# Performance work log

Measured on AMD Instinct MI355X. Metric: run time of the kernel, lower is better.

Reference implementation:

```python
import math
import jax, jax.numpy as jnp
import numpy as np

# module hyperparams (match init_kwargs)
EMBED = 1024
HEADS = 16
FACTOR = 3  # autocorrelation_factor


def setup_inputs() -> dict:
    key = jax.random.key(0)
    ks = jax.random.split(key, 9)
    B, T, E = 8, 4096, EMBED
    s = 1.0 / np.sqrt(E)
    inp = {"hidden_states": jax.random.normal(ks[0], (B, T, E), jnp.float32)}
    for i, n in enumerate(["q", "k", "v", "o"]):
        inp[f"W{n}"] = jax.random.normal(ks[1 + i], (E, E), jnp.float32) * s
        inp[f"b{n}"] = jax.random.normal(ks[5 + i], (E,), jnp.float32) * 0.01
    return inp


def reference(hidden_states, Wq, bq, Wk, bk, Wv, bv, Wo, bo):
    B, T, E = hidden_states.shape
    H = HEADS
    D = E // H  # head_dim

    def shape(x):  # [B,T,E] -> [B*H, T, D]
        return x.reshape(B, T, H, D).transpose(0, 2, 1, 3).reshape(B * H, T, D)

    q = shape(hidden_states @ Wq + bq)
    k = shape(hidden_states @ Wk + bk)
    v = shape(hidden_states @ Wv + bv)

    # FFT-based autocorrelation along the time axis: irfft(rfft(Q) * conj(rfft(K)))
    qf = jnp.fft.rfft(q, axis=1)
    kf = jnp.fft.rfft(k, axis=1)
    attn_weights = jnp.fft.irfft(qf * jnp.conj(kf), n=T, axis=1)  # [B*H, T, D]

    # mean over heads and channel -> [B, T]
    mean_ac = attn_weights.reshape(B, H, T, D).mean(axis=(1, 3))
    top_k = int(FACTOR * math.log(T))
    top_vals, top_idx = jax.lax.top_k(mean_ac, top_k)  # [B, K] each
    # NOTE: original code computes softmax of top_vals but (typo:
    # `top_k_autocrrelations`) never uses it; the raw autocorrelation values
    # are used as aggregation weights. We replicate that exactly.

    BN = B * H
    # torch `.repeat(num_heads, ...)` on a [bsz,1,1] tensor tiles the bsz block
    # num_heads times, so flat index bn maps to batch bn % B.
    bidx = jnp.arange(BN) % B
    w_flat = top_vals[bidx]  # [BN, K]
    d_flat = top_idx[bidx]   # [BN, K]

    t = jnp.arange(T)

    def body(acc, kd):
        d_k, w_k = kd  # [BN], [BN]
        # gather from doubled values == circular shift by delay
        idx = (t[None, :] + d_k[:, None]) % T  # [BN, T]
        rolled = jnp.take_along_axis(v, idx[:, :, None], axis=1)  # [BN, T, D]
        return acc + w_k[:, None, None] * rolled, None

    agg, _ = jax.lax.scan(body, jnp.zeros_like(v), (d_flat.T, w_flat.T))

    out = agg.reshape(B, H, T, D).transpose(0, 2, 1, 3).reshape(B, T, E)
    return out @ Wo + bo
```

## Files before the change

### kernel.cpp

```cpp
#include <hip/hip_runtime.h>


typedef unsigned short u16;
typedef __attribute__((ext_vector_type(8))) short short8_t;
typedef __attribute__((ext_vector_type(4))) float float4_t;

struct cplx { float x, y; };
struct __align__(8) u16x4 { u16 x, y, z, w; };

#define DEVINL static __device__ __forceinline__

DEVINL u16 bf_from_f(float x){
  unsigned u = __float_as_uint(x);
  u += 0x7fffu + ((u >> 16) & 1u);
  return (u16)(u >> 16);
}
DEVINL float f_from_bf(u16 h){ return __uint_as_float(((unsigned)h) << 16); }

DEVINL void nt_store_f(float* p, float v){ __builtin_nontemporal_store(v, p); }
DEVINL void nt_store_u16(u16* p, u16 v){ __builtin_nontemporal_store(v, p); }
DEVINL void nt_store_f4(float* p, float4_t v){ __builtin_nontemporal_store(v, (float4_t*)p); }

typedef const void __attribute__((address_space(1)))* gas_ptr;
typedef void __attribute__((address_space(3)))* las_ptr;
DEVINL void async16(const void* g, void* l){
  __builtin_amdgcn_global_load_lds((gas_ptr)g, (las_ptr)l, 16, 0, 0);
}


__global__ void k_split2(const float* __restrict__ Wq, const float* __restrict__ Wk,
                         u16* __restrict__ Qh, u16* __restrict__ Ql,
                         u16* __restrict__ Kh, u16* __restrict__ Kl){
  int isK = blockIdx.x >> 10;
  int i = (blockIdx.x & 1023) * 256 + threadIdx.x;
  const float* src = isK ? Wk : Wq;
  u16* ph = isK ? Kh : Qh;
  u16* pl = isK ? Kl : Ql;
  float4 v = ((const float4*)src)[i];
  u16x4 h, l;
  h.x = bf_from_f(v.x); l.x = bf_from_f(v.x - f_from_bf(h.x));
  h.y = bf_from_f(v.y); l.y = bf_from_f(v.y - f_from_bf(h.y));
  h.z = bf_from_f(v.z); l.z = bf_from_f(v.z - f_from_bf(h.z));
  h.w = bf_from_f(v.w); l.w = bf_from_f(v.w - f_from_bf(h.w));
  ((u16x4*)ph)[i] = h; ((u16x4*)pl)[i] = l;
}

__global__ void k_transpose2_bf16(const float* __restrict__ Wv, const float* __restrict__ Wo,
                                  u16* __restrict__ WvT, u16* __restrict__ WoT){
  __shared__ float tile[32][33];
  const float* W = blockIdx.z ? Wo : Wv;
  u16* WT = blockIdx.z ? WoT : WvT;
  int k0 = blockIdx.x * 32, n0 = blockIdx.y * 32;
  int x = threadIdx.x, y0 = threadIdx.y;
  for (int j = y0; j < 32; j += 8) tile[j][x] = W[(size_t)(k0 + j) * 1024 + n0 + x];
  __syncthreads();
  for (int j = y0; j < 32; j += 8) WT[(size_t)(n0 + j) * 1024 + k0 + x] = bf_from_f(tile[x][j]);
}

__global__ __launch_bounds__(256) void k_uvc(const float* __restrict__ Wq,
    const float* __restrict__ Wk, const float* __restrict__ bq, const float* __restrict__ bk,
    float* __restrict__ u, float* __restrict__ w2, float* __restrict__ c0){
  int gw = blockIdx.x * 4 + (threadIdx.x >> 6);
  int lane = threadIdx.x & 63;
  if (gw < 2048){
    const float* row = (gw < 1024) ? (Wq + (size_t)gw * 1024) : (Wk + (size_t)(gw - 1024) * 1024);
    const float* vec = (gw < 1024) ? bk : bq;
    float s = 0;
    for (int m = lane; m < 1024; m += 64) s += row[m] * vec[m];
    for (int o = 32; o; o >>= 1) s += __shfl_down(s, o);
    if (lane == 0){ if (gw < 1024) u[gw] = s; else w2[gw - 1024] = s; }
  } else if (gw == 2048){
    float s = 0;
    for (int m = lane; m < 1024; m += 64) s += bq[m] * bk[m];
    for (int o = 32; o; o >>= 1) s += __shfl_down(s, o);
    if (lane == 0) c0[0] = s;
  }
}

__global__ __launch_bounds__(256) void k_prep_hs(const float* __restrict__ hs,
    u16* __restrict__ hi, u16* __restrict__ lo, float* __restrict__ hsT,
    const float* __restrict__ uu, const float* __restrict__ w2,
    float* __restrict__ partQ, float* __restrict__ partK){
  __shared__ float tile[64][66];
  int b = blockIdx.z;
  int t0 = blockIdx.x * 64, e0 = blockIdx.y * 64;
  int tid = threadIdx.x;
  int eq = tid & 15;
  int tr = tid >> 4;
  const float* ib = hs + (size_t)b * 4194304;
  float4 u4 = *(const float4*)(uu + e0 + eq * 4);
  float4 w4 = *(const float4*)(w2 + e0 + eq * 4);
  float a1 = 0.f, a2 = 0.f;
  #pragma unroll
  for (int r = 0; r < 4; ++r){
    int t = tr + r * 16;
    size_t off = (size_t)(t0 + t) * 1024 + e0 + eq * 4;
    float4 v = *(const float4*)(ib + off);
    a1 += v.x * u4.x + v.y * u4.y + v.z * u4.z + v.w * u4.w;
    a2 += v.x * w4.x + v.y * w4.y + v.z * w4.z + v.w * w4.w;
    u16x4 h, l;
    h.x = bf_from_f(v.x); l.x = bf_from_f(v.x - f_from_bf(h.x));
    h.y = bf_from_f(v.y); l.y = bf_from_f(v.y - f_from_bf(h.y));
    h.z = bf_from_f(v.z); l.z = bf_from_f(v.z - f_from_bf(h.z));
    h.w = bf_from_f(v.w); l.w = bf_from_f(v.w - f_from_bf(h.w));
    size_t goff = (size_t)b * 4194304 + off;
    *(u16x4*)(hi + goff) = h; *(u16x4*)(lo + goff) = l;
    float* tp = &tile[t][eq * 4];
    tp[0] = v.x; tp[1] = v.y; tp[2] = v.z; tp[3] = v.w;
  }
  for (int o = 32; o; o >>= 1){
    a1 += __shfl_down(a1, o);
    a2 += __shfl_down(a2, o);
  }
  if ((tid & 63) == 0){
    int idx = b * 4096 + (blockIdx.x * 16 + blockIdx.y) * 4 + (tid >> 6);
    partQ[idx] = a1; partK[idx] = a2;
  }
  __syncthreads();
  float* ob = hsT + (size_t)b * 4194304;
  int tq = tid & 15;
  int er = tid >> 4;
  #pragma unroll
  for (int r = 0; r < 4; ++r){
    int e = er + r * 16;
    float4_t o4;
    o4.x = tile[tq * 4 + 0][e];
    o4.y = tile[tq * 4 + 1][e];
    o4.z = tile[tq * 4 + 2][e];
    o4.w = tile[tq * 4 + 3][e];
    nt_store_f4(ob + (size_t)(e0 + e) * 4096 + t0 + tq * 4, o4);
  }
}


DEVINL void stage_tile(const u16* __restrict__ src, int ld, int row0, int kb,
                       u16* lds, int wave, int lane){
  int r = lane >> 2, c = lane & 3;
  #pragma unroll
  for (int is = wave; is < 8; is += 4){
    const u16* g = src + (size_t)(row0 + is * 16 + r) * ld + kb + c * 8;
    async16((const void*)g, (void*)(lds + is * 512));
  }
}

template<int SPLIT, int MODE>
DEVINL void gemm_body(const u16* __restrict__ Ah, const u16* __restrict__ Al,
                      const u16* __restrict__ Bh, const u16* __restrict__ Bl,
                      float* __restrict__ outF, u16* __restrict__ outB, u16* __restrict__ outB2,
                      const float* __restrict__ bias, int M, int N, int K,
                      int m0, int n0, u16* sAh, u16* sBh, u16* sAl, u16* sBl)
{
  int tid = threadIdx.x, wave = tid >> 6, lane = tid & 63;
  int wm = wave >> 1, wn = wave & 1;
  float4_t zero = {0.0f, 0.0f, 0.0f, 0.0f};
  float4_t acc[4][4];
  #pragma unroll
  for (int i = 0; i < 4; i++)
    #pragma unroll
    for (int j = 0; j < 4; j++) acc[i][j] = zero;

  int ar = wm * 64 + (lane & 15);
  int bc = wn * 64 + (lane & 15);
  int kq = (lane >> 4) * 8;

  for (int kb = 0; kb < K; kb += 32){
    stage_tile(Ah, K, m0, kb, sAh, wave, lane);
    stage_tile(Bh, K, n0, kb, sBh, wave, lane);
    if (SPLIT){
      stage_tile(Al, K, m0, kb, sAl, wave, lane);
      stage_tile(Bl, K, n0, kb, sBl, wave, lane);
    }
    __syncthreads();
    short8_t af[4], bfr[4], afl[4], bfl[4];
    #pragma unroll
    for (int i = 0; i < 4; i++){
      af[i]  = *(const short8_t*)(sAh + (ar + i * 16) * 32 + kq);
      bfr[i] = *(const short8_t*)(sBh + (bc + i * 16) * 32 + kq);
      if (SPLIT){
        afl[i] = *(const short8_t*)(sAl + (ar + i * 16) * 32 + kq);
        bfl[i] = *(const short8_t*)(sBl + (bc + i * 16) * 32 + kq);
      }
    }
    #pragma unroll
    for (int mi = 0; mi < 4; mi++)
      #pragma unroll
      for (int ni = 0; ni < 4; ni++){
        acc[mi][ni] = __builtin_amdgcn_mfma_f32_16x16x32_bf16(af[mi], bfr[ni], acc[mi][ni], 0, 0, 0);
        if (SPLIT){
          acc[mi][ni] = __builtin_amdgcn_mfma_f32_16x16x32_bf16(af[mi], bfl[ni], acc[mi][ni], 0, 0, 0);
          acc[mi][ni] = __builtin_amdgcn_mfma_f32_16x16x32_bf16(afl[mi], bfr[ni], acc[mi][ni], 0, 0, 0);
        }
      }
    __syncthreads();
  }

  int col = lane & 15, rq = lane >> 4;
  #pragma unroll
  for (int mi = 0; mi < 4; mi++)
    #pragma unroll
    for (int ni = 0; ni < 4; ni++){
      int gm = m0 + wm * 64 + mi * 16 + rq * 4;
      int gn = n0 + wn * 64 + ni * 16 + col;
      float4_t v = acc[mi][ni];
      #pragma unroll
      for (int r = 0; r < 4; r++){
        int row = gm + r;
        if (MODE == 0){
          outF[(size_t)row * N + gn] = v[r];
        } else if (MODE == 1){
          int bb = gn >> 12, t = gn & 4095;
          nt_store_f(&outF[(size_t)bb * 4194304 + (size_t)row * 4096 + t], v[r]);
        } else if (MODE == 2){
          nt_store_u16(&outB[(size_t)row * N + gn], bf_from_f(v[r] + bias[gn]));
        } else if (MODE == 3){
          nt_store_f(&outF[(size_t)row * N + gn], v[r] + bias[gn]);
        } else {
          float val = v[r];
          u16 h = bf_from_f(val);
          outB[(size_t)row * N + gn] = h;
          outB2[(size_t)row * N + gn] = bf_from_f(val - f_from_bf(h));
        }
      }
    }
}

template<int SPLIT, int MODE>
__global__ __launch_bounds__(256) void k_gemm128(
    const u16* __restrict__ Ah, const u16* __restrict__ Al,
    const u16* __restrict__ Bh, const u16* __restrict__ Bl,
    float* __restrict__ outF, u16* __restrict__ outB, u16* __restrict__ outB2,
    const float* __restrict__ bias, int M, int N, int K)
{
  __shared__ u16 sAh[128 * 32];
  __shared__ u16 sBh[128 * 32];
  __shared__ u16 sAl[SPLIT ? 128 * 32 : 8];
  __shared__ u16 sBl[SPLIT ? 128 * 32 : 8];
  gemm_body<SPLIT, MODE>(Ah, Al, Bh, Bl, outF, outB, outB2, bias, M, N, K,
                         blockIdx.y * 128, blockIdx.x * 128, sAh, sBh, sAl, sBl);
}

__global__ __launch_bounds__(256) void k_gemm_pv(
    const u16* __restrict__ At_hi, const u16* __restrict__ At_lo,
    const u16* __restrict__ hs_hi, const u16* __restrict__ hs_lo,
    float* __restrict__ Pt, const u16* __restrict__ WvT, u16* __restrict__ Vb,
    const float* __restrict__ bv)
{
  __shared__ u16 smem[4 * 128 * 32];
  int bx = blockIdx.x;
  if (bx < 2048){
    int x = bx & 7, j = bx >> 3;
    int n = x * 32 + (j >> 3);
    int m = j & 7;
    gemm_body<1, 1>(At_hi, At_lo, hs_hi, hs_lo, Pt, nullptr, nullptr, nullptr,
                    1024, 32768, 1024, m * 128, n * 128,
                    smem, smem + 4096, smem + 8192, smem + 12288);
  } else {
    int id = bx - 2048;
    int x = id & 7, j = id >> 3;
    int m = x * 32 + (j >> 3);
    int n = j & 7;
    gemm_body<0, 2>(hs_hi, nullptr, WvT, nullptr, nullptr, Vb, nullptr, bv,
                    32768, 1024, 1024, m * 128, n * 128,
                    smem, smem + 4096, smem + 8192, smem + 12288);
  }
}


#define FPAD(i) ((i) + ((i) >> 3))

__global__ __launch_bounds__(256) void k_fft_fwd(const float* __restrict__ Pt,
                                                 const float* __restrict__ hsT,
                                                 float* __restrict__ S){
  __shared__ float zr[4608];
  __shared__ float zi[4608];
  int tid = threadIdx.x;
  int b = blockIdx.x >> 7;
  int ch0 = (blockIdx.x & 127) * 8;
  float Gre[8], Gim[8];
  #pragma unroll
  for (int j = 0; j < 8; ++j){ Gre[j] = 0.f; Gim[j] = 0.f; }
  float g0 = 0.f, g1 = 0.f;

  for (int c = 0; c < 8; ++c){
    __syncthreads();
    size_t base = ((size_t)b * 1024 + ch0 + c) * 4096;
    for (int i = tid; i < 4096; i += 256){
      zr[FPAD(i)] = Pt[base + i];
      zi[FPAD(i)] = hsT[base + i];
    }
    for (int h = 1024; h >= 1; h >>= 2){
      __syncthreads();
      float wsc = -3.14159265358979323846f / (float)(2 * h);
      for (int g = tid; g < 1024; g += 256){
        int lo = g & (h - 1);
        int i0 = ((g - lo) << 2) + lo;
        int j0 = FPAD(i0), j1 = FPAD(i0 + h), j2 = FPAD(i0 + 2 * h), j3 = FPAD(i0 + 3 * h);
        float x0 = zr[j0], y0 = zi[j0];
        float x1 = zr[j1], y1 = zi[j1];
        float x2 = zr[j2], y2 = zi[j2];
        float x3 = zr[j3], y3 = zi[j3];
        float s, co;
        __sincosf(wsc * (float)lo, &s, &co);
        float b0x = x0 + x2, b0y = y0 + y2;
        float t2x = x0 - x2, t2y = y0 - y2;
        float b2x = t2x * co - t2y * s, b2y = t2x * s + t2y * co;
        float b1x = x1 + x3, b1y = y1 + y3;
        float t3x = x1 - x3, t3y = y1 - y3;
        float b3x = t3x * s + t3y * co, b3y = t3y * s - t3x * co;
        float vc = co * co - s * s, vs = 2.0f * co * s;
        float d1x = b0x - b1x, d1y = b0y - b1y;
        float d3x = b2x - b3x, d3y = b2y - b3y;
        zr[j0] = b0x + b1x;            zi[j0] = b0y + b1y;
        zr[j1] = d1x * vc - d1y * vs;  zi[j1] = d1x * vs + d1y * vc;
        zr[j2] = b2x + b3x;            zi[j2] = b2y + b3y;
        zr[j3] = d3x * vc - d3y * vs;  zi[j3] = d3x * vs + d3y * vc;
      }
    }
    __syncthreads();
    #pragma unroll
    for (int j = 0; j < 8; ++j){
      int idx = tid + (j << 8);
      if (idx < 2047){
        int m = idx + 1;
        int e = 31 - __clz(m);
        int p = m + (1 << e);
        int q = (3 << (e + 1)) - 1 - p;
        int ip = FPAD(p), iq = FPAD(q);
        float xa = zr[ip], ya = zi[ip];
        float xb = zr[iq], yb = zi[iq];
        Gre[j] += 0.5f * (xa * yb + ya * xb);
        Gim[j] += 0.25f * ((xa * xa + ya * ya) - (xb * xb + yb * yb));
      }
    }
    if (tid == 0){
      g0 += zr[0] * zi[0];
      g1 += zr[FPAD(1)] * zi[FPAD(1)];
    }
  }

  float* Sb = S + (size_t)b * 2049 * 2;
  #pragma unroll
  for (int j = 0; j < 8; ++j){
    int idx = tid + (j << 8);
    if (idx < 2047){
      atomicAdd(&Sb[(2 + idx) * 2], Gre[j]);
      atomicAdd(&Sb[(2 + idx) * 2 + 1], Gim[j]);
    }
  }
  if (tid == 0){ atomicAdd(&Sb[0], g0); atomicAdd(&Sb[2], g1); }
}

__global__ __launch_bounds__(256) void k_fft_inv_topk(const float* __restrict__ S,
    const float* __restrict__ partQ, const float* __restrict__ partK,
    const float* __restrict__ c0, float* __restrict__ tv, int* __restrict__ ti){
  __shared__ cplx z[4096];
  __shared__ float vals[4096];
  __shared__ float rv[256];
  __shared__ int ri[256];
  __shared__ float sred[8];
  int b = blockIdx.x, tid = threadIdx.x;
  {
    const float* pQ = partQ + (size_t)b * 4096;
    const float* pK = partK + (size_t)b * 4096;
    float aq = 0.f, ak = 0.f;
    for (int i = tid; i < 4096; i += 256){ aq += pQ[i]; ak += pK[i]; }
    for (int o = 32; o; o >>= 1){ aq += __shfl_down(aq, o); ak += __shfl_down(ak, o); }
    if ((tid & 63) == 0){ sred[tid >> 6] = aq; sred[4 + (tid >> 6)] = ak; }
  }
  const float* Sb = S + (size_t)b * 2049 * 2;
  #pragma unroll
  for (int j = 0; j < 8; ++j){
    int idx = tid + (j << 8);
    if (idx < 2047){
      int m = idx + 1;
      int e = 31 - __clz(m);
      int p = m + (1 << e);
      int q = (3 << (e + 1)) - 1 - p;
      float re = Sb[(2 + idx) * 2], im = Sb[(2 + idx) * 2 + 1];
      z[p].x = re; z[p].y = -im;
      z[q].x = re; z[q].y = im;
    }
  }
  if (tid == 0){
    z[0].x = Sb[0]; z[0].y = -Sb[1];
    z[1].x = Sb[2]; z[1].y = -Sb[3];
  }
  for (int d = 1; d <= 2048; d <<= 1){
    __syncthreads();
    for (int j = tid; j < 2048; j += 256){
      int lo = j & (d - 1);
      int i = ((j & ~(d - 1)) << 1) | lo;
      float ang = -3.14159265358979323846f * (float)lo / (float)d;
      float s, co;
      __sincosf(ang, &s, &co);
      cplx av = z[i], bv = z[i + d];
      float tx = bv.x * co - bv.y * s;
      float ty = bv.x * s + bv.y * co;
      z[i].x = av.x + tx;     z[i].y = av.y + ty;
      z[i + d].x = av.x - tx; z[i + d].y = av.y - ty;
    }
  }
  __syncthreads();
  float Sqb = sred[0] + sred[1] + sred[2] + sred[3];
  float Skb = sred[4] + sred[5] + sred[6] + sred[7];
  float constv = (Sqb + Skb + 4096.0f * c0[0]) * (1.0f / 1024.0f);
  for (int t = tid; t < 4096; t += 256)
    vals[t] = z[t].x * (1.0f / 4194304.0f) + constv;
  __syncthreads();
  for (int it = 0; it < 24; ++it){
    float best = -3.0e38f; int bi = 0x7fffffff;
    for (int i = tid; i < 4096; i += 256){
      float v = vals[i];
      if (v > best){ best = v; bi = i; }
    }
    rv[tid] = best; ri[tid] = bi;
    __syncthreads();
    for (int s = 128; s > 0; s >>= 1){
      if (tid < s){
        if (rv[tid + s] > rv[tid] || (rv[tid + s] == rv[tid] && ri[tid + s] < ri[tid])){
          rv[tid] = rv[tid + s]; ri[tid] = ri[tid + s];
        }
      }
      __syncthreads();
    }
    if (tid == 0){
      tv[b * 24 + it] = rv[0]; ti[b * 24 + it] = ri[0];
      vals[ri[0]] = -3.0e38f;
    }
    __syncthreads();
  }
}


__global__ __launch_bounds__(256, 4) void k_aggregate(const u16* __restrict__ V,
    const float* __restrict__ tv, const int* __restrict__ ti, u16* __restrict__ agg){
  __shared__ float wv[8][24];
  __shared__ int dv[8][24];
  int tid = threadIdx.x;
  if (tid < 192){ int s = tid / 24, k = tid % 24; wv[s][k] = tv[tid]; dv[s][k] = ti[tid]; }
  __syncthreads();
  int flat = blockIdx.x;
  int b = flat & 7;
  int t0 = (flat >> 3) * 16;
  int oct = tid & 127;
  int th = tid >> 7;
  int e = oct * 8;
  int sb = (oct >> 3) & 7;
  const u16* Vbase = V + (size_t)b * 4194304 + e;
  u16* abase = agg + (size_t)b * 4194304 + e;

  float wk[24]; int dk[24];
  #pragma unroll
  for (int k = 0; k < 24; ++k){ wk[k] = wv[sb][k]; dk[k] = dv[sb][k]; }

  for (int tt = 0; tt < 8; ++tt){
    int t = t0 + tt * 2 + th;
    float a0 = 0, a1 = 0, a2 = 0, a3 = 0, a4 = 0, a5 = 0, a6 = 0, a7 = 0;
    #pragma unroll
    for (int k = 0; k < 24; ++k){
      int st = (t + dk[k]) & 4095;
      int4 vv = *(const int4*)(Vbase + (size_t)st * 1024);
      float w = wk[k];
      a0 += w * __uint_as_float(((unsigned)vv.x) << 16);
      a1 += w * __uint_as_float(((unsigned)vv.x) & 0xFFFF0000u);
      a2 += w * __uint_as_float(((unsigned)vv.y) << 16);
      a3 += w * __uint_as_float(((unsigned)vv.y) & 0xFFFF0000u);
      a4 += w * __uint_as_float(((unsigned)vv.z) << 16);
      a5 += w * __uint_as_float(((unsigned)vv.z) & 0xFFFF0000u);
      a6 += w * __uint_as_float(((unsigned)vv.w) << 16);
      a7 += w * __uint_as_float(((unsigned)vv.w) & 0xFFFF0000u);
    }
    int4 o;
    o.x = (int)((unsigned)bf_from_f(a0) | ((unsigned)bf_from_f(a1) << 16));
    o.y = (int)((unsigned)bf_from_f(a2) | ((unsigned)bf_from_f(a3) << 16));
    o.z = (int)((unsigned)bf_from_f(a4) | ((unsigned)bf_from_f(a5) << 16));
    o.w = (int)((unsigned)bf_from_f(a6) | ((unsigned)bf_from_f(a7) << 16));
    *(int4*)(abase + (size_t)t * 1024) = o;
  }
}


extern "C" void kernel_launch(void* const* d_in, const int* in_sizes, int n_in,
                              void* d_out, int out_size, void* d_ws, size_t ws_size,
                              hipStream_t stream){
  const float* hs = (const float*)d_in[0];
  const float* Wq = (const float*)d_in[1];
  const float* bq = (const float*)d_in[2];
  const float* Wk = (const float*)d_in[3];
  const float* bk = (const float*)d_in[4];
  const float* Wv = (const float*)d_in[5];
  const float* bv = (const float*)d_in[6];
  const float* Wo = (const float*)d_in[7];
  const float* bo = (const float*)d_in[8];

  char* ws = (char*)d_ws;
  const size_t MB = 1024ull * 1024ull;
  u16* hs_hi = (u16*)(ws);
  u16* hs_lo = (u16*)(ws + 64 * MB);
  float* Pt  = (float*)(ws + 128 * MB);
  float* hsT = (float*)(ws + 256 * MB);
  u16* Vb    = (u16*)(ws + 384 * MB);
  char* sm   = ws + 448 * MB;
  u16* Wq_hi = (u16*)(sm + 0 * MB);
  u16* Wq_lo = (u16*)(sm + 2 * MB);
  u16* Wk_hi = (u16*)(sm + 4 * MB);
  u16* Wk_lo = (u16*)(sm + 6 * MB);
  u16* WvT   = (u16*)(sm + 8 * MB);
  u16* WoT   = (u16*)(sm + 10 * MB);
  float* partQ = (float*)(sm + 12 * MB);
  float* partK = (float*)(sm + 13 * MB);
  u16* At_hi = (u16*)(sm + 16 * MB);
  u16* At_lo = (u16*)(sm + 18 * MB);
  float* S   = (float*)(sm + 20 * MB);
  float* uu  = (float*)(sm + 22 * MB);
  float* w2  = (float*)(sm + 22 * MB + 8192);
  float* c0  = (float*)(sm + 22 * MB + 16384);
  float* tv  = (float*)(sm + 22 * MB + 17152);
  int*   ti  = (int*)(sm + 22 * MB + 18176);
  u16* agg   = hs_hi;

  hipMemsetAsync(S, 0, 8 * 2049 * 2 * sizeof(float), stream);

  k_uvc<<<513, 256, 0, stream>>>(Wq, Wk, bq, bk, uu, w2, c0);
  k_split2<<<2048, 256, 0, stream>>>(Wq, Wk, Wq_hi, Wq_lo, Wk_hi, Wk_lo);
  k_transpose2_bf16<<<dim3(32, 32, 2), dim3(32, 8), 0, stream>>>(Wv, Wo, WvT, WoT);
  k_prep_hs<<<dim3(64, 16, 8), 256, 0, stream>>>(hs, hs_hi, hs_lo, hsT, uu, w2, partQ, partK);

  k_gemm128<1, 4><<<dim3(8, 8), 256, 0, stream>>>(Wk_hi, Wk_lo, Wq_hi, Wq_lo,
                                                  nullptr, At_hi, At_lo, nullptr, 1024, 1024, 1024);
  k_gemm_pv<<<4096, 256, 0, stream>>>(At_hi, At_lo, hs_hi, hs_lo, Pt, WvT, Vb, bv);

  k_fft_fwd<<<1024, 256, 0, stream>>>(Pt, hsT, S);
  k_fft_inv_topk<<<8, 256, 0, stream>>>(S, partQ, partK, c0, tv, ti);
  k_aggregate<<<2048, 256, 0, stream>>>(Vb, tv, ti, agg);
  k_gemm128<0, 3><<<dim3(8, 256), 256, 0, stream>>>(agg, nullptr, WoT, nullptr,
                                                    (float*)d_out, nullptr, nullptr, bo, 32768, 1024, 1024);
}
```

Before: 1.095 ms.

## Register-blocked radix-16 FFT passes and fuse weight prep kernels into one launch

The forward FFT now keeps 16 points per thread in registers and runs two radix-4 stages per pass. That cuts the per-channel transform from six LDS-round-trip stages with syncs to three register-resident passes with fewer shared-memory reads, writes and barriers. The input load goes straight from global memory into registers before the first two stages. Separately, the three weight-prep kernels (split, transpose, bias dot products) merge into a single launch to save launch overhead. The cost is higher register pressure in the FFT kernel, which may lower occupancy.

```diff
diff --git a/kernel.cpp b/kernel.cpp
--- a/kernel.cpp
+++ b/kernel.cpp
@@ -27,53 +27,55 @@
   __builtin_amdgcn_global_load_lds((gas_ptr)g, (las_ptr)l, 16, 0, 0);
 }
 
-
-__global__ void k_split2(const float* __restrict__ Wq, const float* __restrict__ Wk,
-                         u16* __restrict__ Qh, u16* __restrict__ Ql,
-                         u16* __restrict__ Kh, u16* __restrict__ Kl){
-  int isK = blockIdx.x >> 10;
-  int i = (blockIdx.x & 1023) * 256 + threadIdx.x;
-  const float* src = isK ? Wk : Wq;
-  u16* ph = isK ? Kh : Qh;
-  u16* pl = isK ? Kl : Ql;
-  float4 v = ((const float4*)src)[i];
-  u16x4 h, l;
-  h.x = bf_from_f(v.x); l.x = bf_from_f(v.x - f_from_bf(h.x));
-  h.y = bf_from_f(v.y); l.y = bf_from_f(v.y - f_from_bf(h.y));
-  h.z = bf_from_f(v.z); l.z = bf_from_f(v.z - f_from_bf(h.z));
-  h.w = bf_from_f(v.w); l.w = bf_from_f(v.w - f_from_bf(h.w));
-  ((u16x4*)ph)[i] = h; ((u16x4*)pl)[i] = l;
-}
-
-__global__ void k_transpose2_bf16(const float* __restrict__ Wv, const float* __restrict__ Wo,
-                                  u16* __restrict__ WvT, u16* __restrict__ WoT){
+__global__ __launch_bounds__(256) void k_prep_w(
+    const float* __restrict__ Wq, const float* __restrict__ Wk,
+    const float* __restrict__ bq, const float* __restrict__ bk,
+    u16* __restrict__ Qh, u16* __restrict__ Ql,
+    u16* __restrict__ Kh, u16* __restrict__ Kl,
+    const float* __restrict__ Wv, const float* __restrict__ Wo,
+    u16* __restrict__ WvT, u16* __restrict__ WoT,
+    float* __restrict__ uu, float* __restrict__ w2, float* __restrict__ c0){
   __shared__ float tile[32][33];
-  const float* W = blockIdx.z ? Wo : Wv;
-  u16* WT = blockIdx.z ? WoT : WvT;
-  int k0 = blockIdx.x * 32, n0 = blockIdx.y * 32;
-  int x = threadIdx.x, y0 = threadIdx.y;
-  for (int j = y0; j < 32; j += 8) tile[j][x] = W[(size_t)(k0 + j) * 1024 + n0 + x];
-  __syncthreads();
-  for (int j = y0; j < 32; j += 8) WT[(size_t)(n0 + j) * 1024 + k0 + x] = bf_from_f(tile[x][j]);
-}
-
-__global__ __launch_bounds__(256) void k_uvc(const float* __restrict__ Wq,
-    const float* __restrict__ Wk, const float* __restrict__ bq, const float* __restrict__ bk,
-    float* __restrict__ u, float* __restrict__ w2, float* __restrict__ c0){
-  int gw = blockIdx.x * 4 + (threadIdx.x >> 6);
-  int lane = threadIdx.x & 63;
-  if (gw < 2048){
-    const float* row = (gw < 1024) ? (Wq + (size_t)gw * 1024) : (Wk + (size_t)(gw - 1024) * 1024);
-    const float* vec = (gw < 1024) ? bk : bq;
-    float s = 0;
-    for (int m = lane; m < 1024; m += 64) s += row[m] * vec[m];
-    for (int o = 32; o; o >>= 1) s += __shfl_down(s, o);
-    if (lane == 0){ if (gw < 1024) u[gw] = s; else w2[gw - 1024] = s; }
-  } else if (gw == 2048){
-    float s = 0;
-    for (int m = lane; m < 1024; m += 64) s += bq[m] * bk[m];
-    for (int o = 32; o; o >>= 1) s += __shfl_down(s, o);
-    if (lane == 0) c0[0] = s;
+  int bx = blockIdx.x, tid = threadIdx.x;
+  if (bx < 2048){
+    int isK = bx >> 10;
+    int i = (bx & 1023) * 256 + tid;
+    const float* src = isK ? Wk : Wq;
+    u16* ph = isK ? Kh : Qh;
+    u16* pl = isK ? Kl : Ql;
+    float4 v = ((const float4*)src)[i];
+    u16x4 h, l;
+    h.x = bf_from_f(v.x); l.x = bf_from_f(v.x - f_from_bf(h.x));
+    h.y = bf_from_f(v.y); l.y = bf_from_f(v.y - f_from_bf(h.y));
+    h.z = bf_from_f(v.z); l.z = bf_from_f(v.z - f_from_bf(h.z));
+    h.w = bf_from_f(v.w); l.w = bf_from_f(v.w - f_from_bf(h.w));
+    ((u16x4*)ph)[i] = h; ((u16x4*)pl)[i] = l;
+  } else if (bx < 4096){
+    int id = bx - 2048;
+    const float* W = (id >> 10) ? Wo : Wv;
+    u16* WT = (id >> 10) ? WoT : WvT;
+    int xy = id & 1023;
+    int k0 = (xy & 31) * 32, n0 = (xy >> 5) * 32;
+    int x = tid & 31, y0 = tid >> 5;
+    for (int j = y0; j < 32; j += 8) tile[j][x] = W[(size_t)(k0 + j) * 1024 + n0 + x];
+    __syncthreads();
+    for (int j = y0; j < 32; j += 8) WT[(size_t)(n0 + j) * 1024 + k0 + x] = bf_from_f(tile[x][j]);
+  } else {
+    int gw = (bx - 4096) * 4 + (tid >> 6);
+    int lane = tid & 63;
+    if (gw < 2048){
+      const float* row = (gw < 1024) ? (Wq + (size_t)gw * 1024) : (Wk + (size_t)(gw - 1024) * 1024);
+      const float* vec = (gw < 1024) ? bk : bq;
+      float s = 0;
+      for (int m = lane; m < 1024; m += 64) s += row[m] * vec[m];
+      for (int o = 32; o; o >>= 1) s += __shfl_down(s, o);
+      if (lane == 0){ if (gw < 1024) uu[gw] = s; else w2[gw - 1024] = s; }
+    } else if (gw == 2048){
+      float s = 0;
+      for (int m = lane; m < 1024; m += 64) s += bq[m] * bk[m];
+      for (int o = 32; o; o >>= 1) s += __shfl_down(s, o);
+      if (lane == 0) c0[0] = s;
+    }
   }
 }
 
@@ -268,6 +270,26 @@
 
 #define FPAD(i) ((i) + ((i) >> 3))
 
+DEVINL void bf4(float& x0, float& y0, float& x1, float& y1,
+                float& x2, float& y2, float& x3, float& y3,
+                float s, float co){
+  float b0x = x0 + x2, b0y = y0 + y2;
+  float t2x = x0 - x2, t2y = y0 - y2;
+  float b2x = t2x * co - t2y * s, b2y = t2x * s + t2y * co;
+  float b1x = x1 + x3, b1y = y1 + y3;
+  float t3x = x1 - x3, t3y = y1 - y3;
+  float b3x = t3x * s + t3y * co, b3y = t3y * s - t3x * co;
+  float vc = co * co - s * s, vs = 2.0f * co * s;
+  float d1x = b0x - b1x, d1y = b0y - b1y;
+  float d3x = b2x - b3x, d3y = b2y - b3y;
+  x0 = b0x + b1x;           y0 = b0y + b1y;
+  x1 = d1x * vc - d1y * vs; y1 = d1x * vs + d1y * vc;
+  x2 = b2x + b3x;           y2 = b2y + b3y;
+  x3 = d3x * vc - d3y * vs; y3 = d3x * vs + d3y * vc;
+}
+
+#define PI_F 3.14159265358979323846f
+
 __global__ __launch_bounds__(256) void k_fft_fwd(const float* __restrict__ Pt,
                                                  const float* __restrict__ hsT,
                                                  float* __restrict__ S){
@@ -282,39 +304,101 @@
   float g0 = 0.f, g1 = 0.f;
 
   for (int c = 0; c < 8; ++c){
-    __syncthreads();
     size_t base = ((size_t)b * 1024 + ch0 + c) * 4096;
-    for (int i = tid; i < 4096; i += 256){
-      zr[FPAD(i)] = Pt[base + i];
-      zi[FPAD(i)] = hsT[base + i];
-    }
-    for (int h = 1024; h >= 1; h >>= 2){
-      __syncthreads();
-      float wsc = -3.14159265358979323846f / (float)(2 * h);
-      for (int g = tid; g < 1024; g += 256){
-        int lo = g & (h - 1);
-        int i0 = ((g - lo) << 2) + lo;
-        int j0 = FPAD(i0), j1 = FPAD(i0 + h), j2 = FPAD(i0 + 2 * h), j3 = FPAD(i0 + 3 * h);
-        float x0 = zr[j0], y0 = zi[j0];
-        float x1 = zr[j1], y1 = zi[j1];
-        float x2 = zr[j2], y2 = zi[j2];
-        float x3 = zr[j3], y3 = zi[j3];
+    float xr[4][4], xi[4][4];
+    #pragma unroll
+    for (int a = 0; a < 4; ++a)
+      #pragma unroll
+      for (int bb = 0; bb < 4; ++bb){
+        int i = tid + a * 1024 + bb * 256;
+        xr[a][bb] = Pt[base + i];
+        xi[a][bb] = hsT[base + i];
+      }
+    #pragma unroll
+    for (int bb = 0; bb < 4; ++bb){
+      float s, co;
+      __sincosf(-PI_F * (float)(tid + 256 * bb) * (1.0f / 2048.0f), &s, &co);
+      bf4(xr[0][bb], xi[0][bb], xr[1][bb], xi[1][bb],
+          xr[2][bb], xi[2][bb], xr[3][bb], xi[3][bb], s, co);
+    }
+    {
+      float s, co;
+      __sincosf(-PI_F * (float)tid * (1.0f / 512.0f), &s, &co);
+      #pragma unroll
+      for (int a = 0; a < 4; ++a)
+        bf4(xr[a][0], xi[a][0], xr[a][1], xi[a][1],
+            xr[a][2], xi[a][2], xr[a][3], xi[a][3], s, co);
+    }
+    __syncthreads();
+    #pragma unroll
+    for (int a = 0; a < 4; ++a)
+      #pragma unroll
+      for (int bb = 0; bb < 4; ++bb){
+        int i = tid + a * 1024 + bb * 256;
+        zr[FPAD(i)] = xr[a][bb]; zi[FPAD(i)] = xi[a][bb];
+      }
+    __syncthreads();
+    {
+      int blk = tid >> 4, lo2 = tid & 15;
+      int i0 = blk * 256 + lo2;
+      #pragma unroll
+      for (int a = 0; a < 4; ++a)
+        #pragma unroll
+        for (int bb = 0; bb < 4; ++bb){
+          int i = i0 + a * 64 + bb * 16;
+          xr[a][bb] = zr[FPAD(i)]; xi[a][bb] = zi[FPAD(i)];
+        }
+      #pragma unroll
+      for (int bb = 0; bb < 4; ++bb){
         float s, co;
-        __sincosf(wsc * (float)lo, &s, &co);
-        float b0x = x0 + x2, b0y = y0 + y2;
-        float t2x = x0 - x2, t2y = y0 - y2;
-        float b2x = t2x * co - t2y * s, b2y = t2x * s + t2y * co;
-        float b1x = x1 + x3, b1y = y1 + y3;
-        float t3x = x1 - x3, t3y = y1 - y3;
-        float b3x = t3x * s + t3y * co, b3y = t3y * s - t3x * co;
-        float vc = co * co - s * s, vs = 2.0f * co * s;
-        float d1x = b0x - b1x, d1y = b0y - b1y;
-        float d3x = b2x - b3x, d3y = b2y - b3y;
-        zr[j0] = b0x + b1x;            zi[j0] = b0y + b1y;
-        zr[j1] = d1x * vc - d1y * vs;  zi[j1] = d1x * vs + d1y * vc;
-        zr[j2] = b2x + b3x;            zi[j2] = b2y + b3y;
-        zr[j3] = d3x * vc - d3y * vs;  zi[j3] = d3x * vs + d3y * vc;
-      }
+        __sincosf(-PI_F * (float)(lo2 + 16 * bb) * (1.0f / 128.0f), &s, &co);
+        bf4(xr[0][bb], xi[0][bb], xr[1][bb], xi[1][bb],
+            xr[2][bb], xi[2][bb], xr[3][bb], xi[3][bb], s, co);
+      }
+      {
+        float s, co;
+        __sincosf(-PI_F * (float)lo2 * (1.0f / 32.0f), &s, &co);
+        #pragma unroll
+        for (int a = 0; a < 4; ++a)
+          bf4(xr[a][0], xi[a][0], xr[a][1], xi[a][1],
+              xr[a][2], xi[a][2], xr[a][3], xi[a][3], s, co);
+      }
+      #pragma unroll
+      for (int a = 0; a < 4; ++a)
+        #pragma unroll
+        for (int bb = 0; bb < 4; ++bb){
+          int i = i0 + a * 64 + bb * 16;
+          zr[FPAD(i)] = xr[a][bb]; zi[FPAD(i)] = xi[a][bb];
+        }
+    }
+    __syncthreads();
+    {
+      int i0 = tid * 16;
+      #pragma unroll
+      for (int a = 0; a < 4; ++a)
+        #pragma unroll
+        for (int bb = 0; bb < 4; ++bb){
+          int i = i0 + a * 4 + bb;
+          xr[a][bb] = zr[FPAD(i)]; xi[a][bb] = zi[FPAD(i)];
+        }
+      #pragma unroll
+      for (int bb = 0; bb < 4; ++bb){
+        float s, co;
+        __sincosf(-PI_F * (float)bb * (1.0f / 8.0f), &s, &co);
+        bf4(xr[0][bb], xi[0][bb], xr[1][bb], xi[1][bb],
+            xr[2][bb], xi[2][bb], xr[3][bb], xi[3][bb], s, co);
+      }
+      #pragma unroll
+      for (int a = 0; a < 4; ++a)
+        bf4(xr[a][0], xi[a][0], xr[a][1], xi[a][1],
+            xr[a][2], xi[a][2], xr[a][3], xi[a][3], 0.0f, 1.0f);
+      #pragma unroll
+      for (int a = 0; a < 4; ++a)
+        #pragma unroll
+        for (int bb = 0; bb < 4; ++bb){
+          int i = i0 + a * 4 + bb;
+          zr[FPAD(i)] = xr[a][bb]; zi[FPAD(i)] = xi[a][bb];
+        }
     }
     __syncthreads();
     #pragma unroll
@@ -390,7 +474,7 @@
     for (int j = tid; j < 2048; j += 256){
       int lo = j & (d - 1);
       int i = ((j & ~(d - 1)) << 1) | lo;
-      float ang = -3.14159265358979323846f * (float)lo / (float)d;
+      float ang = -PI_F * (float)lo / (float)d;
       float s, co;
       __sincosf(ang, &s, &co);
       cplx av = z[i], bv = z[i + d];
@@ -521,9 +605,8 @@
 
   hipMemsetAsync(S, 0, 8 * 2049 * 2 * sizeof(float), stream);
 
-  k_uvc<<<513, 256, 0, stream>>>(Wq, Wk, bq, bk, uu, w2, c0);
-  k_split2<<<2048, 256, 0, stream>>>(Wq, Wk, Wq_hi, Wq_lo, Wk_hi, Wk_lo);
-  k_transpose2_bf16<<<dim3(32, 32, 2), dim3(32, 8), 0, stream>>>(Wv, Wo, WvT, WoT);
+  k_prep_w<<<4609, 256, 0, stream>>>(Wq, Wk, bq, bk, Wq_hi, Wq_lo, Wk_hi, Wk_lo,
+                                     Wv, Wo, WvT, WoT, uu, w2, c0);
   k_prep_hs<<<dim3(64, 16, 8), 256, 0, stream>>>(hs, hs_hi, hs_lo, hsT, uu, w2, partQ, partK);
 
   k_gemm128<1, 4><<<dim3(8, 8), 256, 0, stream>>>(Wk_hi, Wk_lo, Wq_hi, Wq_lo,
```

Measured after the change: 1.154 ms. 5.4% more time.
